# Optimization experiments

Measured on AMD Instinct MI355X. Metric: run time of the kernel, lower is better.

The kernel has to match this reference:

```python
import jax, jax.numpy as jnp
import numpy as np

WEIGHT = 0.2
EPS_MAG = 1e-8   # sqrt eps in magnitude
EPS_NORM = 1e-12 # F.normalize default eps
EPS_COS = 1e-8   # F.cosine_similarity default eps


def _sobel_kernels(C, dtype):
    smooth = np.array([1.0, 2.0, 1.0], np.float32)
    deriv = np.array([-1.0, 0.0, 1.0], np.float32)
    kx = np.einsum('d,h,w->dhw', smooth, smooth, deriv)
    ky = np.einsum('d,h,w->dhw', smooth, deriv, smooth)
    kz = np.einsum('d,h,w->dhw', deriv, smooth, smooth)
    # depthwise kernels: OIDHW with O=C, I=1 (feature_group_count=C)
    return [jnp.asarray(np.broadcast_to(k[None, None], (C, 1, 3, 3, 3)).copy(), dtype)
            for k in (kx, ky, kz)]


def _grads(x, kernels):
    C = x.shape[1]
    dn = jax.lax.conv_dimension_numbers(x.shape, kernels[0].shape,
                                        ('NCDHW', 'OIDHW', 'NCDHW'))
    return [jax.lax.conv_general_dilated(x, k, window_strides=(1, 1, 1),
                                         padding=[(1, 1)] * 3,
                                         dimension_numbers=dn,
                                         feature_group_count=C)
            for k in kernels]


def setup_inputs() -> dict:
    key = jax.random.key(0)
    k1, k2 = jax.random.split(key)
    shape = (2, 1, 160, 160, 160)
    return {
        'pred': jax.random.normal(k1, shape, dtype=jnp.float32),
        'target': jax.random.normal(k2, shape, dtype=jnp.float32),
    }


def reference(pred, target):
    C = pred.shape[1]
    kernels = _sobel_kernels(C, pred.dtype)
    pg = jnp.stack(_grads(pred, kernels), axis=1)    # (B, 3, C, D, H, W)
    tg = jnp.stack(_grads(target, kernels), axis=1)  # (B, 3, C, D, H, W)

    pred_mag = jnp.sqrt(jnp.sum(pg * pg, axis=1) + EPS_MAG)
    targ_mag = jnp.sqrt(jnp.sum(tg * tg, axis=1) + EPS_MAG)
    magnitude_loss = jnp.mean((pred_mag - targ_mag) ** 2)

    # F.normalize(p=2, dim=1): x / max(||x||, eps)
    pn = pg / jnp.maximum(jnp.linalg.norm(pg, axis=1, keepdims=True), EPS_NORM)
    tn = tg / jnp.maximum(jnp.linalg.norm(tg, axis=1, keepdims=True), EPS_NORM)

    # F.cosine_similarity(dim=1): dot / (max(||a||,eps) * max(||b||,eps))
    dot = jnp.sum(pn * tn, axis=1)
    na = jnp.maximum(jnp.linalg.norm(pn, axis=1), EPS_COS)
    nb = jnp.maximum(jnp.linalg.norm(tn, axis=1), EPS_COS)
    direction_loss = 1.0 - jnp.mean(dot / (na * nb))

    return WEIGHT * (magnitude_loss + direction_loss)
```

## Files before the change

kernel.cpp:

```cpp
#include <hip/hip_runtime.h>


constexpr int Dd = 160, Hh = 160, Ww = 160;
constexpr int TW = 32, TH = 16, DC = 16;
constexpr int NTX = Ww / TW;
constexpr int NTY = Hh / TH;
constexpr int NTZ = Dd / DC;
constexpr int NBLOCKS = NTX * NTY * NTZ * 2;
constexpr int NXCD = 8;
constexpr int CHUNK = NBLOCKS / NXCD;
constexpr int PLANES = DC + 2;
constexpr int PLSZ = Hh * Ww;
constexpr double NVOX = 2.0 * Dd * Hh * Ww;

constexpr int CROWS = TH + 2;
constexpr int CGP   = 17;
constexpr int NITEM = CROWS * 8;

typedef float v2 __attribute__((ext_vector_type(2)));
typedef float v4 __attribute__((ext_vector_type(4)));
typedef float v4a __attribute__((ext_vector_type(4), aligned(4)));
typedef float v2a __attribute__((ext_vector_type(2), aligned(4)));

__global__ __launch_bounds__(256)
void acl_partial(const float* __restrict__ pred, const float* __restrict__ targ,
                 float2* __restrict__ partial)
{
    __shared__ v4 cmb[2][2][CROWS][CGP];
    __shared__ float rred[8];

    const int tid = threadIdx.x;
    const int gx  = tid & 15;
    const int r   = tid >> 4;

    const int bid = blockIdx.x;
    const int swz = (bid % NXCD) * CHUNK + bid / NXCD;
    const int zt  = swz % NTZ;
    const int t1  = swz / NTZ;
    const int wt  = t1 % NTX;
    const int t2  = t1 / NTX;
    const int ht  = t2 % NTY;
    const int b   = t2 / NTY;

    const int x0 = wt * TW, y0 = ht * TH;
    const int z0 = zt * DC;
    const size_t base = (size_t)b * ((size_t)Dd * PLSZ);
    const float* __restrict__ pv = pred + base;
    const float* __restrict__ tv = targ + base;

    const bool hasItem = (tid < NITEM);
    const int crow = tid >> 3;
    const int cg   = tid & 7;
    const int gyc  = y0 - 1 + crow;
    const bool yokc = hasItem && (gyc >= 0) && (gyc < Hh);
    int gycl = gyc < 0 ? 0 : (gyc > Hh - 1 ? Hh - 1 : gyc);
    const bool fixLo = (x0 == 0) && (cg == 0);
    const bool fixHi = (x0 + TW == Ww) && (cg == 7);
    const int xb = x0 + 4 * cg - 1;
    const int a4 = gycl * Ww + (fixLo ? 0 : xb);
    const int a2 = gycl * Ww + (fixHi ? (Ww - 2) : (xb + 4));

    const v2 z2 = {0.f, 0.f};
    const v4 z4 = {0.f, 0.f, 0.f, 0.f};

    v2 P1x = z2, P1y = z2, P1z = z2, P2x = z2, P2y = z2, P2z = z2;
    v2 T1x = z2, T1y = z2, T1z = z2, T2x = z2, T2y = z2, T2z = z2;
    v2 accm = z2, accc = z2;

    v4 pr4 = z4, tr4 = z4;
    v2 pr2 = z2, tr2 = z2;

    auto issueG = [&](int p2) {
        if (hasItem) {
            int gz = z0 - 1 + p2;
            gz = gz < 0 ? 0 : (gz > Dd - 1 ? Dd - 1 : gz);
            const float* pz = pv + (ptrdiff_t)gz * PLSZ;
            const float* tz = tv + (ptrdiff_t)gz * PLSZ;
            pr4 = *(const v4a*)(pz + a4);  pr2 = *(const v2a*)(pz + a2);
            tr4 = *(const v4a*)(tz + a4);  tr2 = *(const v2a*)(tz + a2);
        }
    };

    auto comboOne = [&](const v4 v, const v2 u, v4& w0, v4& w1) {
        float e0, e1, e2, e3, e4, e5;
        if (fixLo)      { e0 = 0.f;  e1 = v.x; e2 = v.y; e3 = v.z; e4 = v.w; e5 = u.y; }
        else if (fixHi) { e0 = v.x;  e1 = v.y; e2 = v.z; e3 = v.w; e4 = u.y; e5 = 0.f; }
        else            { e0 = v.x;  e1 = v.y; e2 = v.z; e3 = v.w; e4 = u.x; e5 = u.y; }
        const float HS0 = e0 + 2.f*e1 + e2, HS1 = e1 + 2.f*e2 + e3;
        const float HS2 = e2 + 2.f*e3 + e4, HS3 = e3 + 2.f*e4 + e5;
        w0 = (v4){HS0, HS1, e2 - e0, e3 - e1};
        w1 = (v4){HS2, HS3, e4 - e2, e5 - e3};
    };

    auto comboWrite = [&](int p1, int slot) {
        const bool zokc = ((unsigned)(z0 - 1 + p1) < (unsigned)Dd);
        const bool valid = zokc && yokc;
        v4 w0, w1;
        comboOne(pr4, pr2, w0, w1);
        if (!valid) { w0 = z4; w1 = z4; }
        if (hasItem) {
            cmb[slot][0][crow][2 * cg]     = w0;
            cmb[slot][0][crow][2 * cg + 1] = w1;
        }
        comboOne(tr4, tr2, w0, w1);
        if (!valid) { w0 = z4; w1 = z4; }
        if (hasItem) {
            cmb[slot][1][crow][2 * cg]     = w0;
            cmb[slot][1][crow][2 * cg + 1] = w1;
        }
    };

    auto consume = [&](int p, int s) {
        {
            const v4 qm = cmb[s][0][r][gx], q0 = cmb[s][0][r + 1][gx], qp = cmb[s][0][r + 2][gx];
            const v2 A = qm.xy + 2.f*q0.xy + qp.xy;
            const v2 B = qm.zw + 2.f*q0.zw + qp.zw;
            const v2 C = qp.xy - qm.xy;
            const v2 fpx = P1x + B, fpy = P1y + C, fpz = A - P1z;
            P1x = 2.f*B + P2x;  P1y = 2.f*C + P2y;  P1z = P2z;
            P2x = B;  P2y = C;  P2z = A;
            const v4 sm_ = cmb[s][1][r][gx], s0_ = cmb[s][1][r + 1][gx], sp_ = cmb[s][1][r + 2][gx];
            const v2 At = sm_.xy + 2.f*s0_.xy + sp_.xy;
            const v2 Bt = sm_.zw + 2.f*s0_.zw + sp_.zw;
            const v2 Ct = sp_.xy - sm_.xy;
            const v2 ftx = T1x + Bt, fty = T1y + Ct, ftz = At - T1z;
            T1x = 2.f*Bt + T2x;  T1y = 2.f*Ct + T2y;  T1z = T2z;
            T2x = Bt;  T2y = Ct;  T2z = At;

            if (p >= 2) {
                const v2 np2 = fpx*fpx + fpy*fpy + fpz*fpz;
                const v2 nt2 = ftx*ftx + fty*fty + ftz*ftz;
                const v2 a  = np2 + 1e-8f;
                const v2 bb = nt2 + 1e-8f;
                const v2 ab = a * bb;
                v2 rt;
                rt.x = __builtin_amdgcn_sqrtf(ab.x);
                rt.y = __builtin_amdgcn_sqrtf(ab.y);
                accm += a + bb - 2.f*rt;
                const v2 dt = fpx*ftx + fpy*fty + fpz*ftz;
                v2 pr = np2 * nt2;
                pr.x = fmaxf(pr.x, 1e-30f);
                pr.y = fmaxf(pr.y, 1e-30f);
                v2 rq;
                rq.x = __builtin_amdgcn_rsqf(pr.x);
                rq.y = __builtin_amdgcn_rsqf(pr.y);
                accc += dt * rq;
            }
        }
    };

    issueG(0);
    comboWrite(0, 0);
    issueG(1);
    __syncthreads();

    #pragma unroll 1
    for (int p = 0; p < PLANES; ++p) {
        const int s = p & 1;

        consume(p, s);

        if (p + 1 < PLANES) comboWrite(p + 1, s ^ 1);
        if (p + 2 < PLANES) issueG(p + 2);

        __syncthreads();
    }

    float am = accm.x + accm.y;
    float ac = accc.x + accc.y;
    #pragma unroll
    for (int off = 32; off >= 1; off >>= 1) {
        am += __shfl_down(am, off);
        ac += __shfl_down(ac, off);
    }
    const int wid = tid >> 6;
    if ((tid & 63) == 0) { rred[wid] = am; rred[4 + wid] = ac; }
    __syncthreads();
    if (tid == 0) {
        const float m = rred[0] + rred[1] + rred[2] + rred[3];
        const float c = rred[4] + rred[5] + rred[6] + rred[7];
        partial[bid] = make_float2(m, c);
    }
}

__global__ __launch_bounds__(256)
void acl_final(const float2* __restrict__ partial, float* __restrict__ out)
{
    __shared__ double sm[256], sc[256];
    double m = 0.0, c = 0.0;
    for (int i = threadIdx.x; i < NBLOCKS; i += 256) {
        const float2 v = partial[i];
        m += (double)v.x;
        c += (double)v.y;
    }
    sm[threadIdx.x] = m;
    sc[threadIdx.x] = c;
    __syncthreads();
    #pragma unroll
    for (int s = 128; s >= 1; s >>= 1) {
        if (threadIdx.x < (unsigned)s) {
            sm[threadIdx.x] += sm[threadIdx.x + s];
            sc[threadIdx.x] += sc[threadIdx.x + s];
        }
        __syncthreads();
    }
    if (threadIdx.x == 0) {
        const double mag_loss = sm[0] / NVOX;
        const double dir_loss = 1.0 - sc[0] / NVOX;
        out[0] = (float)(0.2 * (mag_loss + dir_loss));
    }
}

extern "C" void kernel_launch(void* const* d_in, const int* in_sizes, int n_in,
                              void* d_out, int out_size, void* d_ws, size_t ws_size,
                              hipStream_t stream) {
    const float* pred = (const float*)d_in[0];
    const float* targ = (const float*)d_in[1];
    float* out = (float*)d_out;
    float2* partial = (float2*)d_ws;

    acl_partial<<<NBLOCKS, 256, 0, stream>>>(pred, targ, partial);
    acl_final<<<1, 256, 0, stream>>>(partial, out);
}
```

Before: 29.45 us.

## Process two z-planes per barrier with four-slot LDS ring and deeper prefetch

```diff
diff --git a/kernel.cpp b/kernel.cpp
--- a/kernel.cpp
+++ b/kernel.cpp
@@ -26,7 +26,7 @@
 void acl_partial(const float* __restrict__ pred, const float* __restrict__ targ,
                  float2* __restrict__ partial)
 {
-    __shared__ v4 cmb[2][2][CROWS][CGP];
+    __shared__ v4 cmb[4][2][CROWS][CGP];
     __shared__ float rred[8];
 
     const int tid = threadIdx.x;
@@ -67,17 +67,17 @@
     v2 T1x = z2, T1y = z2, T1z = z2, T2x = z2, T2y = z2, T2z = z2;
     v2 accm = z2, accc = z2;
 
-    v4 pr4 = z4, tr4 = z4;
-    v2 pr2 = z2, tr2 = z2;
-
-    auto issueG = [&](int p2) {
+    v4 pA4 = z4, tA4 = z4, pB4 = z4, tB4 = z4;
+    v2 pA2 = z2, tA2 = z2, pB2 = z2, tB2 = z2;
+
+    auto issueG = [&](v4& q4, v2& q2, v4& s4, v2& s2, int p2) {
         if (hasItem) {
             int gz = z0 - 1 + p2;
             gz = gz < 0 ? 0 : (gz > Dd - 1 ? Dd - 1 : gz);
             const float* pz = pv + (ptrdiff_t)gz * PLSZ;
             const float* tz = tv + (ptrdiff_t)gz * PLSZ;
-            pr4 = *(const v4a*)(pz + a4);  pr2 = *(const v2a*)(pz + a2);
-            tr4 = *(const v4a*)(tz + a4);  tr2 = *(const v2a*)(tz + a2);
+            q4 = *(const v4a*)(pz + a4);  q2 = *(const v2a*)(pz + a2);
+            s4 = *(const v4a*)(tz + a4);  s2 = *(const v2a*)(tz + a2);
         }
     };
 
@@ -92,17 +92,18 @@
         w1 = (v4){HS2, HS3, e4 - e2, e5 - e3};
     };
 
-    auto comboWrite = [&](int p1, int slot) {
+    auto comboWrite = [&](const v4 q4, const v2 q2, const v4 s4, const v2 s2,
+                          int p1, int slot) {
         const bool zokc = ((unsigned)(z0 - 1 + p1) < (unsigned)Dd);
         const bool valid = zokc && yokc;
         v4 w0, w1;
-        comboOne(pr4, pr2, w0, w1);
+        comboOne(q4, q2, w0, w1);
         if (!valid) { w0 = z4; w1 = z4; }
         if (hasItem) {
             cmb[slot][0][crow][2 * cg]     = w0;
             cmb[slot][0][crow][2 * cg + 1] = w1;
         }
-        comboOne(tr4, tr2, w0, w1);
+        comboOne(s4, s2, w0, w1);
         if (!valid) { w0 = z4; w1 = z4; }
         if (hasItem) {
             cmb[slot][1][crow][2 * cg]     = w0;
@@ -111,57 +112,60 @@
     };
 
     auto consume = [&](int p, int s) {
-        {
-            const v4 qm = cmb[s][0][r][gx], q0 = cmb[s][0][r + 1][gx], qp = cmb[s][0][r + 2][gx];
-            const v2 A = qm.xy + 2.f*q0.xy + qp.xy;
-            const v2 B = qm.zw + 2.f*q0.zw + qp.zw;
-            const v2 C = qp.xy - qm.xy;
-            const v2 fpx = P1x + B, fpy = P1y + C, fpz = A - P1z;
-            P1x = 2.f*B + P2x;  P1y = 2.f*C + P2y;  P1z = P2z;
-            P2x = B;  P2y = C;  P2z = A;
-            const v4 sm_ = cmb[s][1][r][gx], s0_ = cmb[s][1][r + 1][gx], sp_ = cmb[s][1][r + 2][gx];
-            const v2 At = sm_.xy + 2.f*s0_.xy + sp_.xy;
-            const v2 Bt = sm_.zw + 2.f*s0_.zw + sp_.zw;
-            const v2 Ct = sp_.xy - sm_.xy;
-            const v2 ftx = T1x + Bt, fty = T1y + Ct, ftz = At - T1z;
-            T1x = 2.f*Bt + T2x;  T1y = 2.f*Ct + T2y;  T1z = T2z;
-            T2x = Bt;  T2y = Ct;  T2z = At;
-
-            if (p >= 2) {
-                const v2 np2 = fpx*fpx + fpy*fpy + fpz*fpz;
-                const v2 nt2 = ftx*ftx + fty*fty + ftz*ftz;
-                const v2 a  = np2 + 1e-8f;
-                const v2 bb = nt2 + 1e-8f;
-                const v2 ab = a * bb;
-                v2 rt;
-                rt.x = __builtin_amdgcn_sqrtf(ab.x);
-                rt.y = __builtin_amdgcn_sqrtf(ab.y);
-                accm += a + bb - 2.f*rt;
-                const v2 dt = fpx*ftx + fpy*fty + fpz*ftz;
-                v2 pr = np2 * nt2;
-                pr.x = fmaxf(pr.x, 1e-30f);
-                pr.y = fmaxf(pr.y, 1e-30f);
-                v2 rq;
-                rq.x = __builtin_amdgcn_rsqf(pr.x);
-                rq.y = __builtin_amdgcn_rsqf(pr.y);
-                accc += dt * rq;
-            }
-        }
-    };
-
-    issueG(0);
-    comboWrite(0, 0);
-    issueG(1);
+        const v4 qm = cmb[s][0][r][gx], q0 = cmb[s][0][r + 1][gx], qp = cmb[s][0][r + 2][gx];
+        const v2 A = qm.xy + 2.f*q0.xy + qp.xy;
+        const v2 B = qm.zw + 2.f*q0.zw + qp.zw;
+        const v2 C = qp.xy - qm.xy;
+        const v2 fpx = P1x + B, fpy = P1y + C, fpz = A - P1z;
+        P1x = 2.f*B + P2x;  P1y = 2.f*C + P2y;  P1z = P2z;
+        P2x = B;  P2y = C;  P2z = A;
+
+        const v4 sm_ = cmb[s][1][r][gx], s0_ = cmb[s][1][r + 1][gx], sp_ = cmb[s][1][r + 2][gx];
+        const v2 At = sm_.xy + 2.f*s0_.xy + sp_.xy;
+        const v2 Bt = sm_.zw + 2.f*s0_.zw + sp_.zw;
+        const v2 Ct = sp_.xy - sm_.xy;
+        const v2 ftx = T1x + Bt, fty = T1y + Ct, ftz = At - T1z;
+        T1x = 2.f*Bt + T2x;  T1y = 2.f*Ct + T2y;  T1z = T2z;
+        T2x = Bt;  T2y = Ct;  T2z = At;
+
+        if (p >= 2) {
+            const v2 np2 = fpx*fpx + fpy*fpy + fpz*fpz;
+            const v2 nt2 = ftx*ftx + fty*fty + ftz*ftz;
+            const v2 a  = np2 + 1e-8f;
+            const v2 bb = nt2 + 1e-8f;
+            const v2 ab = a * bb;
+            v2 rt;
+            rt.x = __builtin_amdgcn_sqrtf(ab.x);
+            rt.y = __builtin_amdgcn_sqrtf(ab.y);
+            accm += a + bb - 2.f*rt;
+            const v2 dt = fpx*ftx + fpy*fty + fpz*ftz;
+            v2 pr = np2 * nt2;
+            pr.x = fmaxf(pr.x, 1e-30f);
+            pr.y = fmaxf(pr.y, 1e-30f);
+            v2 rq;
+            rq.x = __builtin_amdgcn_rsqf(pr.x);
+            rq.y = __builtin_amdgcn_rsqf(pr.y);
+            accc += dt * rq;
+        }
+    };
+
+    issueG(pA4, pA2, tA4, tA2, 0);
+    issueG(pB4, pB2, tB4, tB2, 1);
+    comboWrite(pA4, pA2, tA4, tA2, 0, 0);
+    comboWrite(pB4, pB2, tB4, tB2, 1, 1);
+    issueG(pA4, pA2, tA4, tA2, 2);
+    issueG(pB4, pB2, tB4, tB2, 3);
     __syncthreads();
 
     #pragma unroll 1
-    for (int p = 0; p < PLANES; ++p) {
-        const int s = p & 1;
-
-        consume(p, s);
-
-        if (p + 1 < PLANES) comboWrite(p + 1, s ^ 1);
-        if (p + 2 < PLANES) issueG(p + 2);
+    for (int pp = 0; pp < PLANES; pp += 2) {
+        consume(pp,     pp & 3);
+        consume(pp + 1, (pp + 1) & 3);
+
+        if (pp + 2 < PLANES) comboWrite(pA4, pA2, tA4, tA2, pp + 2, (pp + 2) & 3);
+        if (pp + 3 < PLANES) comboWrite(pB4, pB2, tB4, tB2, pp + 3, (pp + 3) & 3);
+        if (pp + 4 < PLANES) issueG(pA4, pA2, tA4, tA2, pp + 4);
+        if (pp + 5 < PLANES) issueG(pB4, pB2, tB4, tB2, pp + 5);
 
         __syncthreads();
     }
```

New measurement: 28.91 us. About the same (-1.8%).
